# Kernel optimization log

Measured on AMD Instinct MI355X. Metric: run time of the kernel, lower is better.

The kernel has to match this reference:

```python
import jax
import jax.numpy as jnp
import numpy as np

VOCAB = 16384
WIDTH = 256
BETA = 0.25
EPS = 1e-12  # F.normalize eps


def setup_inputs() -> dict:
    key = jax.random.key(0)
    k1, k2, k3 = jax.random.split(key, 3)
    class_tokens = jax.random.normal(k1, (32, 1, WIDTH), dtype=jnp.float32)
    patch_tokens = jax.random.normal(k2, (32, WIDTH, 16, 16), dtype=jnp.float32)
    W = jax.random.normal(k3, (VOCAB, WIDTH), dtype=jnp.float32) * 0.02  # codebook
    return {"class_tokens": class_tokens, "patch_tokens": patch_tokens, "W": W}


def _l2norm(x):
    return x / jnp.maximum(jnp.linalg.norm(x, axis=-1, keepdims=True), EPS)


def reference(class_tokens, patch_tokens, W):
    B, L, C = class_tokens.shape
    _, _, H, Wd = patch_tokens.shape
    # (B,C,H,W) -> (B,HW,C)
    pt = patch_tokens.reshape(B, C, H * Wd).transpose(0, 2, 1)
    NxC = jnp.concatenate([class_tokens, pt], axis=1).reshape(-1, C)  # [N,C]

    # vocab_norm branch: cosine-similarity argmax on detached, normalized vectors
    xn = _l2norm(jax.lax.stop_gradient(NxC))      # [N,C]
    Wn = _l2norm(W)                                # [V,C] (column-normalized W.T)
    sim = xn @ Wn.T                                # [N,V] big matmul
    idx = jnp.argmax(sim, axis=1)                  # [N]

    counts = jnp.zeros((VOCAB,), jnp.float32).at[idx].add(1.0)  # bincount

    fhat_g = W[idx]                                # codebook gather [N,C]
    vq_loss = BETA * jnp.mean((jax.lax.stop_gradient(fhat_g) - NxC) ** 2) \
              + jnp.mean((fhat_g - jax.lax.stop_gradient(NxC)) ** 2)

    # straight-through estimator
    fhat = jax.lax.stop_gradient(fhat_g - NxC) + NxC

    prob = counts / counts.sum()
    vocab_usage = jnp.mean((prob > 0.01 / VOCAB).astype(jnp.float32)) * 100.0

    fhat = fhat.reshape(B, L + H * Wd, C)
    fhat_class = fhat[:, :L, :]
    fhat_patch = fhat[:, L:, :].reshape(B, H, Wd, C).transpose(0, 3, 1, 2)
    return fhat_class, fhat_patch, vq_loss, vocab_usage
```

## Files before the change

### kernel.cpp

```cpp
#include <hip/hip_runtime.h>
#include <stdint.h>

#define VOCAB 16384
#define NB 32
#define NTOK 8224
#define MTILES 65
#define MP 8320
#define NBY 128
#define TILE_BYTES 65536
#define PHASE_BYTES 16384
#define NLOSS 2056
#define MWIN 2.25e-3f
#define TOKCHUNKS 520

typedef _Float16 half8 __attribute__((ext_vector_type(8)));
typedef float f4 __attribute__((ext_vector_type(4)));
typedef __attribute__((address_space(1))) const uint32_t* gas_t;
typedef __attribute__((address_space(3))) uint32_t* las_t;

__device__ __forceinline__ void async16(const void* g, void* l) {
    __builtin_amdgcn_global_load_lds((gas_t)g, (las_t)l, 16, 0, 0);
}

__device__ __forceinline__ unsigned long long key64(float v, int idx) {
    unsigned u = __float_as_uint(v);
    u = (u & 0x80000000u) ? ~u : (u | 0x80000000u);
    return ((unsigned long long)u << 32) | (unsigned)(~idx);
}

__device__ __forceinline__ float keyval(unsigned long long k) {
    unsigned u = (unsigned)(k >> 32);
    u = (u & 0x80000000u) ? (u & 0x7fffffffu) : ~u;
    return __uint_as_float(u);
}

__device__ __forceinline__ void merge2(unsigned long long& k1, unsigned long long& k2,
                                       unsigned long long p1, unsigned long long p2) {
    unsigned long long lo = k1 < p1 ? k1 : p1;
    k1 = k1 > p1 ? k1 : p1;
    unsigned long long m2 = k2 > p2 ? k2 : p2;
    k2 = lo > m2 ? lo : m2;
}

__global__ __launch_bounds__(256) void k_patch(const float* __restrict__ patch, float* __restrict__ tok) {
    __shared__ float t[64][65];
    int c0 = blockIdx.x * 64, p0 = blockIdx.y * 64, b = blockIdx.z;
    int tid = threadIdx.x;
    int l = tid & 63, w = tid >> 6;
    const float* src = patch + b * 65536;
#pragma unroll
    for (int i = 0; i < 16; ++i) {
        int row = i * 4 + w;
        t[row][l] = src[(c0 + row) * 256 + p0 + l];
    }
    __syncthreads();
#pragma unroll
    for (int i = 0; i < 16; ++i) {
        int prow = i * 4 + w;
        tok[(b * 257 + 1 + p0 + prow) * 256 + c0 + l] = t[l][prow];
    }
}

__global__ __launch_bounds__(256) void k_pack2(const float* __restrict__ tok, const float* __restrict__ cls,
                                               const float* __restrict__ W, char* __restrict__ apk,
                                               char* __restrict__ bpk, float* __restrict__ ntokv,
                                               float* __restrict__ nwv) {
    __shared__ float t[16][264];
    __shared__ float pr[16][16];
    __shared__ float sn[16];
    int g0 = blockIdx.x;
    bool isTok = g0 < TOKCHUNKS;
    int g = isTok ? g0 : g0 - TOKCHUNKS;
    char* dst = isTok ? apk : bpk;
    float* norms = isTok ? ntokv : nwv;
    int nrows = isTok ? NTOK : VOCAB;
    int row0 = g * 16;
    int tid = threadIdx.x;
    int rr = tid >> 4, cb = tid & 15;
    int grow = row0 + rr;
    const float* sp;
    if (isTok) {
        int b = grow / 257, s = grow - b * 257;
        sp = (s == 0) ? (cls + (size_t)b * 256 + cb * 16) : (tok + (size_t)grow * 256 + cb * 16);
    } else {
        sp = W + (size_t)grow * 256 + cb * 16;
    }
    float psum = 0.0f;
#pragma unroll
    for (int i = 0; i < 4; ++i) {
        float4 v = (grow < nrows) ? *(const float4*)(sp + i * 4) : make_float4(0.f, 0.f, 0.f, 0.f);
        *(float4*)&t[rr][cb * 16 + i * 4] = v;
        psum += v.x * v.x + v.y * v.y + v.z * v.z + v.w * v.w;
    }
    pr[rr][cb] = psum;
    __syncthreads();
    if (tid < 16) {
        float s = 0.0f;
#pragma unroll
        for (int j = 0; j < 16; ++j) s += pr[tid][j];
        float nv = fmaxf(sqrtf(s), 1e-12f);
        sn[tid] = nv;
        norms[row0 + tid] = nv;
    }
    __syncthreads();
    int c = tid & 63, pair = tid >> 6;
    int m = c & 15, jb = (c >> 4) * 8;
    float inv = 1.0f / sn[m];
    char* base = dst + (size_t)(g >> 3) * TILE_BYTES + (size_t)(g & 7) * 1024 + c * 16;
#pragma unroll
    for (int it = 0; it < 2; ++it) {
        int k32 = it * 4 + pair;
        const float* rowp = &t[m][k32 * 32 + jb];
        half8 o;
#pragma unroll
        for (int j = 0; j < 8; ++j) o[j] = (_Float16)(rowp[j] * inv);
        *(half8*)(base + (size_t)k32 * 8192) = o;
    }
}

__global__ __launch_bounds__(256) void k_sim(const char* __restrict__ apk, const char* __restrict__ bpk,
                                             unsigned long long* __restrict__ pb) {
    __shared__ char lds[65536];
    int id = blockIdx.x;
    int xcd = id & 7, r = id >> 3;
    int st = r / 104, within = r % 104;
    int stid = xcd * 10 + st;
    int sx = stid % 5, sy = stid / 5;
    int bx = sx * 13 + within % 13;
    int by = sy * 8 + within / 13;

    int tid = threadIdx.x;
    int ln = tid & 63, wv = tid >> 6;
    int mh = wv >> 1, nh = wv & 1;
    const char* abase = apk + (size_t)bx * TILE_BYTES;
    const half8* Bg = (const half8*)(bpk + (size_t)by * TILE_BYTES);

    f4 acc[4][4];
#pragma unroll
    for (int i = 0; i < 4; ++i)
#pragma unroll
        for (int j = 0; j < 4; ++j) acc[i][j] = (f4){0.f, 0.f, 0.f, 0.f};

    half8 b0[2][4], b1[2][4];
#define LOADB(DST, P)                                                                 \
    _Pragma("unroll")                                                                 \
    for (int s = 0; s < 2; ++s)                                                       \
        _Pragma("unroll")                                                             \
        for (int ni = 0; ni < 4; ++ni)                                                \
            DST[s][ni] = Bg[((P) * 16 + s * 8 + nh * 4 + ni) * 64 + ln];

#define FRAGS(P)                                                                      \
    half8 ah[2][4];                                                                   \
    _Pragma("unroll")                                                                 \
    for (int s = 0; s < 2; ++s) {                                                     \
        const half8* Af = (const half8*)(lds + (P) * 16384 + s * 8192);               \
        _Pragma("unroll")                                                             \
        for (int mi = 0; mi < 4; ++mi) ah[s][mi] = Af[(mh * 4 + mi) * 64 + ln];       \
    }

#define DOMFMA(BH)                                                                    \
    __builtin_amdgcn_s_setprio(1);                                                    \
    _Pragma("unroll")                                                                 \
    for (int s = 0; s < 2; ++s)                                                       \
        _Pragma("unroll")                                                             \
        for (int mi = 0; mi < 4; ++mi)                                                \
            _Pragma("unroll")                                                         \
            for (int ni = 0; ni < 4; ++ni)                                            \
                acc[mi][ni] = __builtin_amdgcn_mfma_f32_16x16x32_f16(BH[s][ni], ah[s][mi], acc[mi][ni], 0, 0, 0); \
    __builtin_amdgcn_s_setprio(0);

    LOADB(b0, 0);
#pragma unroll
    for (int i = 0; i < 16; ++i) {
        int c = wv * 16 + i;
        async16(abase + (c << 10) + (ln << 4), lds + (c << 10));
    }
    LOADB(b1, 1);
    __syncthreads();

    { FRAGS(0); DOMFMA(b0); }
    __builtin_amdgcn_sched_barrier(0);
    { LOADB(b0, 2); FRAGS(1); DOMFMA(b1); }
    __builtin_amdgcn_sched_barrier(0);
    { LOADB(b1, 3); FRAGS(2); DOMFMA(b0); }
    __builtin_amdgcn_sched_barrier(0);
    { FRAGS(3); DOMFMA(b1); }

    __syncthreads();
    unsigned long long* s1 = (unsigned long long*)lds;
    unsigned long long* s2 = (unsigned long long*)(lds + 2048);

    int col = ln & 15, quad = ln >> 4;
    unsigned qb = (unsigned)(3 - quad) << 4;
    int nbase0 = by * 128 + nh * 64;
#pragma unroll
    for (int mi = 0; mi < 4; ++mi) {
        float v1 = -3.0f, v2 = -3.5f;
#pragma unroll
        for (int ni = 0; ni < 4; ++ni)
#pragma unroll
            for (int rg = 0; rg < 4; ++rg) {
                unsigned e = 15u - (unsigned)(ni * 4 + rg);
                float pv = __uint_as_float((__float_as_uint(acc[mi][ni][rg]) & 0xFFFFFFF0u) | e);
                v2 = __builtin_amdgcn_fmed3f(v1, v2, pv);
                v1 = fmaxf(v1, pv);
            }
        float w1 = __uint_as_float((__float_as_uint(v1) & 0xFFFFFFCFu) | qb);
        float w2 = __uint_as_float((__float_as_uint(v2) & 0xFFFFFFCFu) | qb);
        v1 = fmaxf(w1, w2);
        v2 = fminf(w1, w2);
#pragma unroll
        for (int off = 16; off < 64; off <<= 1) {
            float p1 = __shfl_xor(v1, off);
            float p2 = __shfl_xor(v2, off);
            v2 = __builtin_amdgcn_fmed3f(v1, p1, fmaxf(v2, p2));
            v1 = fmaxf(v1, p1);
        }
        if (quad == 0) {
            unsigned u1 = __float_as_uint(v1), u2 = __float_as_uint(v2);
            int q1 = 3 - (int)((u1 >> 4) & 3u), o1 = 15 - (int)(u1 & 15u);
            int q2 = 3 - (int)((u2 >> 4) & 3u), o2 = 15 - (int)(u2 & 15u);
            int n1 = ((o1 >> 2) << 4) + q1 * 4 + (o1 & 3);
            int n2 = ((o2 >> 2) << 4) + q2 * 4 + (o2 & 3);
            int row = mh * 64 + mi * 16 + col;
            s1[row * 2 + nh] = key64(v1, nbase0 + n1);
            s2[row * 2 + nh] = key64(v2, nbase0 + n2);
        }
    }
    __syncthreads();
    if (tid < 128) {
        unsigned long long k1 = s1[tid * 2], k2 = s2[tid * 2];
        merge2(k1, k2, s1[tid * 2 + 1], s2[tid * 2 + 1]);
        ulonglong2 v; v.x = k1; v.y = k2;
        ((ulonglong2*)pb)[((size_t)bx * 128 + tid) * 128 + by] = v;
    }
#undef LOADB
#undef FRAGS
#undef DOMFMA
}

__global__ __launch_bounds__(256) void k_gather(const unsigned long long* __restrict__ pb,
                                                const float* __restrict__ W, const float* __restrict__ tok,
                                                const float* __restrict__ cls,
                                                const float* __restrict__ ntok, const float* __restrict__ nw,
                                                float* __restrict__ out, int* __restrict__ idxbuf,
                                                float* __restrict__ lossbuf, unsigned int* __restrict__ used) {
    __shared__ float lp[4];
    int tid = threadIdx.x;
    int t = blockIdx.x * 4 + (tid >> 6);
    int ln = tid & 63, w = tid >> 6;
    const ulonglong2* pv = (const ulonglong2*)pb;
    ulonglong2 ea = pv[(size_t)t * 128 + ln];
    ulonglong2 eb = pv[(size_t)t * 128 + 64 + ln];
    unsigned long long g = ea.x > eb.x ? ea.x : eb.x;
#pragma unroll
    for (int off = 1; off < 64; off <<= 1) {
        unsigned long long o = __shfl_xor(g, off);
        if (o > g) g = o;
    }
    float T = keyval(g) - MWIN;
    int tq = t / 257, ts = t - tq * 257;
    const float* xrow = (ts == 0) ? (cls + (size_t)tq * 256) : (tok + (size_t)t * 256);
    f4 xv = *(const f4*)&xrow[ln * 4];
    float nt = ntok[t];
    unsigned long long k4[4] = {ea.x, ea.y, eb.x, eb.y};
    float bestv = -3.0f;
    int besti = 0x7fffffff;
#pragma unroll
    for (int gi = 0; gi < 4; ++gi) {
        unsigned long long mask = __ballot(keyval(k4[gi]) >= T);
        while (mask) {
            int src = __ffsll((unsigned long long)mask) - 1;
            mask &= mask - 1;
            unsigned long long ck = __shfl(k4[gi], src);
            int ci = (int)(~(unsigned)(ck & 0xffffffffu));
            f4 wc = *(const f4*)&W[(size_t)ci * 256 + ln * 4];
            float d = xv.x * wc.x + xv.y * wc.y + xv.z * wc.z + xv.w * wc.w;
#pragma unroll
            for (int off = 1; off < 64; off <<= 1) d += __shfl_xor(d, off);
            float sim = d / (nt * nw[ci]);
            if (sim > bestv || (sim == bestv && ci < besti)) { bestv = sim; besti = ci; }
        }
    }
    int bi = besti;
    f4 wr = *(const f4*)&W[(size_t)bi * 256 + ln * 4];
    float dx = wr.x - xv.x, dy = wr.y - xv.y, dz = wr.z - xv.z, dw = wr.w - xv.w;
    float ls = dx * dx + dy * dy + dz * dz + dw * dw;
#pragma unroll
    for (int off = 1; off < 64; off <<= 1) ls += __shfl_xor(ls, off);
    if (ln == 0) {
        lp[w] = ls;
        atomicOr(&used[bi >> 5], 1u << (bi & 31));
        idxbuf[t] = bi;
    }
    if (ts == 0) {
        *(f4*)&out[tq * 256 + ln * 4] = wr;
    }
    __syncthreads();
    if (tid == 0) lossbuf[blockIdx.x] = lp[0] + lp[1] + lp[2] + lp[3];
}

__global__ __launch_bounds__(256) void k_scatter(const int* __restrict__ idxbuf, const float* __restrict__ W,
                                                 float* __restrict__ out, const unsigned int* __restrict__ used,
                                                 const float* __restrict__ lossbuf) {
    __shared__ float t64[64][65];
    __shared__ int sidx[64];
    int c0 = blockIdx.x * 64, p0 = blockIdx.y * 64, b = blockIdx.z;
    int tid = threadIdx.x;
    if (tid < 64) sidx[tid] = idxbuf[b * 257 + 1 + p0 + tid];
    __syncthreads();
    int l = tid & 63, w = tid >> 6;
#pragma unroll
    for (int i = 0; i < 16; ++i) {
        int p = i * 4 + w;
        t64[p][l] = W[(size_t)sidx[p] * 256 + c0 + l];
    }
    __syncthreads();
#pragma unroll
    for (int i = 0; i < 16; ++i) {
        int c = i * 4 + w;
        out[8192 + (size_t)b * 65536 + (size_t)(c0 + c) * 256 + p0 + l] = t64[l][c];
    }
    if (blockIdx.x == 0 && blockIdx.y == 0 && blockIdx.z == 0) {
        int cnt = 0;
        float ls = 0.0f;
        for (int i = tid; i < VOCAB / 32; i += 256) cnt += __popc(used[i]);
        for (int i = tid; i < NLOSS; i += 256) ls += lossbuf[i];
#pragma unroll
        for (int off = 32; off > 0; off >>= 1) {
            cnt += __shfl_down(cnt, off);
            ls += __shfl_down(ls, off);
        }
        __shared__ int p4f[4];
        __shared__ float f4s[4];
        if ((tid & 63) == 0) { p4f[tid >> 6] = cnt; f4s[tid >> 6] = ls; }
        __syncthreads();
        if (tid == 0) {
            int c = p4f[0] + p4f[1] + p4f[2] + p4f[3];
            float lsum = f4s[0] + f4s[1] + f4s[2] + f4s[3];
            out[8192 + 2097152] = 1.25f * lsum / (float)(NTOK * 256);
            out[8192 + 2097152 + 1] = 100.0f * (float)c / (float)VOCAB;
        }
    }
}

extern "C" void kernel_launch(void* const* d_in, const int* in_sizes, int n_in,
                              void* d_out, int out_size, void* d_ws, size_t ws_size,
                              hipStream_t stream) {
    (void)in_sizes; (void)n_in; (void)out_size; (void)ws_size;
    const float* cls = (const float*)d_in[0];
    const float* patch = (const float*)d_in[1];
    const float* W = (const float*)d_in[2];
    float* out = (float*)d_out;

    char* ws = (char*)d_ws;
    float* tok = (float*)ws;
    char* apk = ws + (size_t)NTOK * 256 * 4;
    char* bpk = apk + (size_t)MTILES * TILE_BYTES;
    unsigned long long* pb = (unsigned long long*)(bpk + (size_t)NBY * TILE_BYTES);
    float* ntokv = (float*)(pb + (size_t)MP * NBY * 2);
    float* nwv = ntokv + MP;
    float* lossbuf = nwv + VOCAB;
    int* idxbuf = (int*)(lossbuf + NLOSS);
    unsigned int* used = (unsigned int*)(idxbuf + NTOK);

    hipMemsetAsync(used, 0, (VOCAB / 32) * sizeof(unsigned int), stream);

    k_patch<<<dim3(4, 4, NB), 256, 0, stream>>>(patch, tok);
    k_pack2<<<TOKCHUNKS + VOCAB / 16, 256, 0, stream>>>(tok, cls, W, apk, bpk, ntokv, nwv);
    k_sim<<<MTILES * NBY, 256, 0, stream>>>(apk, bpk, pb);
    k_gather<<<NLOSS, 256, 0, stream>>>(pb, W, tok, cls, ntokv, nwv, out, idxbuf, lossbuf, used);
    k_scatter<<<dim3(4, 4, NB), 256, 0, stream>>>(idxbuf, W, out, used, lossbuf);
}
```

Measured before the change: 192.9 us.

## Fuse scatter and final reduction into gather kernel, skip rescoring for single candidates

New measurement: 284.6 us. 1.48x slower.

```diff
diff --git a/kernel.cpp b/kernel.cpp
--- a/kernel.cpp
+++ b/kernel.cpp
@@ -8,7 +8,6 @@
 #define MP 8320
 #define NBY 128
 #define TILE_BYTES 65536
-#define PHASE_BYTES 16384
 #define NLOSS 2056
 #define MWIN 2.25e-3f
 #define TOKCHUNKS 520
@@ -232,7 +231,7 @@
         unsigned long long k1 = s1[tid * 2], k2 = s2[tid * 2];
         merge2(k1, k2, s1[tid * 2 + 1], s2[tid * 2 + 1]);
         ulonglong2 v; v.x = k1; v.y = k2;
-        ((ulonglong2*)pb)[((size_t)bx * 128 + tid) * 128 + by] = v;
+        ((ulonglong2*)pb)[((size_t)(bx * 128 + tid)) * 128 + by] = v;
     }
 #undef LOADB
 #undef FRAGS
@@ -243,9 +242,11 @@
                                                 const float* __restrict__ W, const float* __restrict__ tok,
                                                 const float* __restrict__ cls,
                                                 const float* __restrict__ ntok, const float* __restrict__ nw,
-                                                float* __restrict__ out, int* __restrict__ idxbuf,
-                                                float* __restrict__ lossbuf, unsigned int* __restrict__ used) {
+                                                float* __restrict__ out,
+                                                float* __restrict__ lossbuf, unsigned int* __restrict__ used,
+                                                unsigned int* __restrict__ ctr) {
     __shared__ float lp[4];
+    __shared__ int lastflag;
     int tid = threadIdx.x;
     int t = blockIdx.x * 4 + (tid >> 6);
     int ln = tid & 63, w = tid >> 6;
@@ -262,24 +263,40 @@
     int tq = t / 257, ts = t - tq * 257;
     const float* xrow = (ts == 0) ? (cls + (size_t)tq * 256) : (tok + (size_t)t * 256);
     f4 xv = *(const f4*)&xrow[ln * 4];
-    float nt = ntok[t];
     unsigned long long k4[4] = {ea.x, ea.y, eb.x, eb.y};
-    float bestv = -3.0f;
-    int besti = 0x7fffffff;
+    unsigned long long msk[4];
+    int total = 0;
 #pragma unroll
     for (int gi = 0; gi < 4; ++gi) {
-        unsigned long long mask = __ballot(keyval(k4[gi]) >= T);
-        while (mask) {
-            int src = __ffsll((unsigned long long)mask) - 1;
-            mask &= mask - 1;
-            unsigned long long ck = __shfl(k4[gi], src);
-            int ci = (int)(~(unsigned)(ck & 0xffffffffu));
-            f4 wc = *(const f4*)&W[(size_t)ci * 256 + ln * 4];
-            float d = xv.x * wc.x + xv.y * wc.y + xv.z * wc.z + xv.w * wc.w;
-#pragma unroll
-            for (int off = 1; off < 64; off <<= 1) d += __shfl_xor(d, off);
-            float sim = d / (nt * nw[ci]);
-            if (sim > bestv || (sim == bestv && ci < besti)) { bestv = sim; besti = ci; }
+        msk[gi] = __ballot(keyval(k4[gi]) >= T);
+        total += __popcll(msk[gi]);
+    }
+    int besti;
+    if (total == 1) {
+        unsigned long long ck = 0;
+#pragma unroll
+        for (int gi = 0; gi < 4; ++gi)
+            if (msk[gi]) { int src = __ffsll(msk[gi]) - 1; ck = __shfl(k4[gi], src); }
+        besti = (int)(~(unsigned)(ck & 0xffffffffu));
+    } else {
+        float nt = ntok[t];
+        float bestv = -3.0f;
+        besti = 0x7fffffff;
+#pragma unroll
+        for (int gi = 0; gi < 4; ++gi) {
+            unsigned long long mask = msk[gi];
+            while (mask) {
+                int src = __ffsll(mask) - 1;
+                mask &= mask - 1;
+                unsigned long long ck = __shfl(k4[gi], src);
+                int ci = (int)(~(unsigned)(ck & 0xffffffffu));
+                f4 wc = *(const f4*)&W[(size_t)ci * 256 + ln * 4];
+                float d = xv.x * wc.x + xv.y * wc.y + xv.z * wc.z + xv.w * wc.w;
+#pragma unroll
+                for (int off = 1; off < 64; off <<= 1) d += __shfl_xor(d, off);
+                float sim = d / (nt * nw[ci]);
+                if (sim > bestv || (sim == bestv && ci < besti)) { bestv = sim; besti = ci; }
+            }
         }
     }
     int bi = besti;
@@ -291,54 +308,43 @@
     if (ln == 0) {
         lp[w] = ls;
         atomicOr(&used[bi >> 5], 1u << (bi & 31));
-        idxbuf[t] = bi;
     }
     if (ts == 0) {
         *(f4*)&out[tq * 256 + ln * 4] = wr;
-    }
-    __syncthreads();
-    if (tid == 0) lossbuf[blockIdx.x] = lp[0] + lp[1] + lp[2] + lp[3];
-}
-
-__global__ __launch_bounds__(256) void k_scatter(const int* __restrict__ idxbuf, const float* __restrict__ W,
-                                                 float* __restrict__ out, const unsigned int* __restrict__ used,
-                                                 const float* __restrict__ lossbuf) {
-    __shared__ float t64[64][65];
-    __shared__ int sidx[64];
-    int c0 = blockIdx.x * 64, p0 = blockIdx.y * 64, b = blockIdx.z;
-    int tid = threadIdx.x;
-    if (tid < 64) sidx[tid] = idxbuf[b * 257 + 1 + p0 + tid];
-    __syncthreads();
-    int l = tid & 63, w = tid >> 6;
-#pragma unroll
-    for (int i = 0; i < 16; ++i) {
-        int p = i * 4 + w;
-        t64[p][l] = W[(size_t)sidx[p] * 256 + c0 + l];
-    }
-    __syncthreads();
-#pragma unroll
-    for (int i = 0; i < 16; ++i) {
-        int c = i * 4 + w;
-        out[8192 + (size_t)b * 65536 + (size_t)(c0 + c) * 256 + p0 + l] = t64[l][c];
-    }
-    if (blockIdx.x == 0 && blockIdx.y == 0 && blockIdx.z == 0) {
+    } else {
+        float* obase = out + 8192 + (size_t)tq * 65536 + (ts - 1);
+        obase[(4 * ln + 0) * 256] = wr.x;
+        obase[(4 * ln + 1) * 256] = wr.y;
+        obase[(4 * ln + 2) * 256] = wr.z;
+        obase[(4 * ln + 3) * 256] = wr.w;
+    }
+    __syncthreads();
+    if (tid == 0) {
+        lossbuf[blockIdx.x] = lp[0] + lp[1] + lp[2] + lp[3];
+        __threadfence();
+        unsigned prev = atomicAdd(ctr, 1u);
+        lastflag = (prev == NLOSS - 1);
+    }
+    __syncthreads();
+    if (lastflag) {
+        __threadfence();
         int cnt = 0;
-        float ls = 0.0f;
+        float lsum = 0.0f;
         for (int i = tid; i < VOCAB / 32; i += 256) cnt += __popc(used[i]);
-        for (int i = tid; i < NLOSS; i += 256) ls += lossbuf[i];
+        for (int i = tid; i < NLOSS; i += 256) lsum += lossbuf[i];
 #pragma unroll
         for (int off = 32; off > 0; off >>= 1) {
             cnt += __shfl_down(cnt, off);
-            ls += __shfl_down(ls, off);
+            lsum += __shfl_down(lsum, off);
         }
         __shared__ int p4f[4];
         __shared__ float f4s[4];
-        if ((tid & 63) == 0) { p4f[tid >> 6] = cnt; f4s[tid >> 6] = ls; }
+        if ((tid & 63) == 0) { p4f[tid >> 6] = cnt; f4s[tid >> 6] = lsum; }
         __syncthreads();
         if (tid == 0) {
             int c = p4f[0] + p4f[1] + p4f[2] + p4f[3];
-            float lsum = f4s[0] + f4s[1] + f4s[2] + f4s[3];
-            out[8192 + 2097152] = 1.25f * lsum / (float)(NTOK * 256);
+            float l = f4s[0] + f4s[1] + f4s[2] + f4s[3];
+            out[8192 + 2097152] = 1.25f * l / (float)(NTOK * 256);
             out[8192 + 2097152 + 1] = 100.0f * (float)c / (float)VOCAB;
         }
     }
@@ -361,14 +367,13 @@
     float* ntokv = (float*)(pb + (size_t)MP * NBY * 2);
     float* nwv = ntokv + MP;
     float* lossbuf = nwv + VOCAB;
-    int* idxbuf = (int*)(lossbuf + NLOSS);
-    unsigned int* used = (unsigned int*)(idxbuf + NTOK);
-
-    hipMemsetAsync(used, 0, (VOCAB / 32) * sizeof(unsigned int), stream);
+    unsigned int* used = (unsigned int*)(lossbuf + NLOSS);
+    unsigned int* ctr = used + VOCAB / 32;
+
+    hipMemsetAsync(used, 0, (VOCAB / 32 + 1) * sizeof(unsigned int), stream);
 
     k_patch<<<dim3(4, 4, NB), 256, 0, stream>>>(patch, tok);
     k_pack2<<<TOKCHUNKS + VOCAB / 16, 256, 0, stream>>>(tok, cls, W, apk, bpk, ntokv, nwv);
     k_sim<<<MTILES * NBY, 256, 0, stream>>>(apk, bpk, pb);
-    k_gather<<<NLOSS, 256, 0, stream>>>(pb, W, tok, cls, ntokv, nwv, out, idxbuf, lossbuf, used);
-    k_scatter<<<dim3(4, 4, NB), 256, 0, stream>>>(idxbuf, W, out, used, lossbuf);
-}
+    k_gather<<<NLOSS, 256, 0, stream>>>(pb, W, tok, cls, ntokv, nwv, out, lossbuf, used, ctr);
+}
```
